# Optimization experiments

Measured on AMD Instinct MI355X. Metric: run time of the kernel, lower is better.

Reference implementation:

```python
import jax, jax.numpy as jnp
import numpy as np

NUM_EXPERTS = 8
NUM_ROWS = 1024
HIDDEN = 2048
INTER = 1024
TOPK = 2


def setup_inputs() -> dict:
    key = jax.random.key(0)
    kx, kr, k1, k2, k3 = jax.random.split(key, 5)
    x = jax.random.normal(kx, (NUM_ROWS, HIDDEN), dtype=jnp.float32)
    router_probs = jax.random.normal(kr, (NUM_ROWS, NUM_EXPERTS), dtype=jnp.float32)
    fc1 = jax.random.uniform(k1, (NUM_EXPERTS, HIDDEN, INTER), minval=-0.1, maxval=0.1, dtype=jnp.float32)
    fc2 = jax.random.uniform(k2, (NUM_EXPERTS, INTER, HIDDEN), minval=-0.1, maxval=0.1, dtype=jnp.float32)
    fc3 = jax.random.uniform(k3, (NUM_EXPERTS, HIDDEN, INTER), minval=-0.1, maxval=0.1, dtype=jnp.float32)
    return {"x": x, "router_probs": router_probs, "fc1": fc1, "fc2": fc2, "fc3": fc3}


def reference(x, router_probs, fc1, fc2, fc3):
    # Router: softmax over experts, top-k, renormalize
    router_softmax = jax.nn.softmax(router_probs.astype(jnp.float32), axis=1).astype(router_probs.dtype)
    topk_probs, topk_indices = jax.lax.top_k(router_softmax, TOPK)  # [N,K]
    topk_probs = topk_probs / jnp.sum(topk_probs, axis=1, keepdims=True)

    # Per-token combine weight for each expert: w[n,e] = sum_k prob[n,k]*[idx[n,k]==e]
    one_hot = jax.nn.one_hot(topk_indices, NUM_EXPERTS, dtype=x.dtype)  # [N,K,E]
    combine = jnp.einsum("nk,nke->ne", topk_probs, one_hot)  # [N,E]

    # Dense grouped GEMMs over all experts (reference form of dispatch/combine)
    h1 = jnp.einsum("nh,ehi->eni", x, fc1)  # [E,N,I]
    h3 = jnp.einsum("nh,ehi->eni", x, fc3)  # [E,N,I]
    act = jax.nn.silu(h1) * h3  # swiglu
    h2 = jnp.einsum("eni,eih->enh", act, fc2)  # [E,N,H]
    out = jnp.einsum("ne,enh->nh", combine, h2)  # [N,H]
    return out
```

## Files before the change

### kernel.cpp

```cpp
#include <hip/hip_runtime.h>

#define NEXP 8
#define NTOK 1024
#define HID 2048
#define ITR 1024

typedef __attribute__((ext_vector_type(8))) short short8;
typedef __attribute__((ext_vector_type(4))) float f32x4;

__device__ __forceinline__ unsigned short f2bf(float f) {
  unsigned u = __float_as_uint(f);
  u += 0x7fffu + ((u >> 16) & 1u);
  return (unsigned short)(u >> 16);
}

__device__ __forceinline__ void gl_lds16(const void* g, void* l) {
  __builtin_amdgcn_global_load_lds(
      (const __attribute__((address_space(1))) unsigned int*)g,
      (__attribute__((address_space(3))) unsigned int*)l, 16, 0, 0);
}

__global__ __launch_bounds__(256) void k_setup(const float* __restrict__ x,
                                               unsigned int* __restrict__ xb,
                                               float* __restrict__ out) {
  int i = blockIdx.x * 256 + threadIdx.x;
  f32x4 z = {0.f, 0.f, 0.f, 0.f};
  *(f32x4*)(out + (size_t)i * 4) = z;
  f32x4 v = *(const f32x4*)(x + (size_t)i * 4);
  xb[(size_t)i * 2] = (unsigned)f2bf(v[0]) | ((unsigned)f2bf(v[1]) << 16);
  xb[(size_t)i * 2 + 1] = (unsigned)f2bf(v[2]) | ((unsigned)f2bf(v[3]) << 16);
}

__global__ __launch_bounds__(1024) void k_router(const float* __restrict__ rp,
                                                 int* __restrict__ counts,
                                                 int* __restrict__ base,
                                                 int* __restrict__ toklist,
                                                 float* __restrict__ wlist) {
  __shared__ int c[NEXP];
  __shared__ int sb[NEXP];
  int n = threadIdx.x;
  if (n < NEXP) c[n] = 0;
  __syncthreads();
  float r[NEXP];
#pragma unroll
  for (int e = 0; e < NEXP; ++e) r[e] = rp[n * NEXP + e];
  int i1 = 0;
  float m1 = r[0];
#pragma unroll
  for (int e = 1; e < NEXP; ++e)
    if (r[e] > m1) { m1 = r[e]; i1 = e; }
  int i2 = -1;
  float m2 = -3.4e38f;
#pragma unroll
  for (int e = 0; e < NEXP; ++e)
    if (e != i1 && r[e] > m2) { m2 = r[e]; i2 = e; }
  float p1 = 1.f / (1.f + __expf(m2 - m1));
  float p2 = 1.f - p1;
  int s1 = atomicAdd(&c[i1], 1);
  int s2 = atomicAdd(&c[i2], 1);
  __syncthreads();
  if (n == 0) {
    int a = 0;
#pragma unroll
    for (int e = 0; e < NEXP; ++e) { sb[e] = a; a += c[e]; }
  }
  __syncthreads();
  int q1 = sb[i1] + s1;
  toklist[q1] = n; wlist[q1] = p1;
  int q2 = sb[i2] + s2;
  toklist[q2] = n; wlist[q2] = p2;
  if (n < NEXP) { counts[n] = c[n]; base[n] = sb[n]; }
}

__global__ __launch_bounds__(256) void k_transcvt(const float* __restrict__ in,
                                                  unsigned short* __restrict__ out,
                                                  int R, int C) {
  const int e = blockIdx.z;
  const float* src = in + (size_t)e * R * C;
  unsigned short* dst = out + (size_t)e * R * C;
  const int r0 = blockIdx.x * 64, c0 = blockIdx.y * 64;
  __shared__ unsigned short t[64][66];
  const int tid = threadIdx.x;
  const int r = tid >> 2, q = tid & 3;
  const float* p = src + (size_t)(r0 + r) * C + c0 + q * 4;
#pragma unroll
  for (int i = 0; i < 4; ++i) {
    f32x4 v = *(const f32x4*)(p + i * 16);
#pragma unroll
    for (int j = 0; j < 4; ++j) t[r][i * 16 + q * 4 + j] = f2bf(v[j]);
  }
  __syncthreads();
  const int cc = tid >> 2, rq = (tid & 3) * 16;
  unsigned short tmp[16];
#pragma unroll
  for (int i = 0; i < 16; ++i) tmp[i] = t[rq + i][cc];
  unsigned short* qo = dst + (size_t)(c0 + cc) * R + r0 + rq;
  *(short8*)qo = *(const short8*)tmp;
  *(short8*)(qo + 8) = *(const short8*)(tmp + 8);
}

__global__ __launch_bounds__(512, 4) void k_gemm13(
    const unsigned short* __restrict__ w1t, const unsigned short* __restrict__ w3t,
    const unsigned short* __restrict__ xb, const int* __restrict__ counts,
    const int* __restrict__ base, const int* __restrict__ toklist,
    unsigned short* __restrict__ act) {
  const int bid = blockIdx.x;
  const int e = bid & 7;
  const int t2 = bid >> 3;
  const int ntile = t2 & 31;
  const int mtile = t2 >> 5;
  const int cnt = counts[e];
  const int mbase = mtile * 256;
  if (mbase >= cnt) return;
  const int n0 = ntile * 32;
  const int rbase = base[e];

  __shared__ __align__(16) unsigned short lds[2 * 20480];
  const int tid = threadIdx.x;
  const int lane = tid & 63, w = tid >> 6;

  const unsigned short* srcA[4];
  int dofA[4];
#pragma unroll
  for (int i = 0; i < 4; ++i) {
    int c = i * 512 + tid;
    int r = c >> 3, b = c & 7;
    int row = mbase + r;
    int tok = toklist[rbase + ((row < cnt) ? row : (cnt - 1))];
    srcA[i] = xb + (size_t)tok * HID + (b ^ (r & 7)) * 8;
    dofA[i] = (i * 512 + w * 64) * 8;
  }
  const int mat = tid >> 8;
  const int cw = tid & 255;
  const int rw = cw >> 3, bw = cw & 7;
  const unsigned short* srcW =
      (mat ? w3t : w1t) + ((size_t)e * ITR + n0 + rw) * HID + (bw ^ (rw & 7)) * 8;
  const int dofW = 16384 + mat * 2048 + (w & 3) * 512;

  int offA[2][2], offW[2][2];
#pragma unroll
  for (int i = 0; i < 2; ++i)
#pragma unroll
    for (int s = 0; s < 2; ++s) {
      int kb = s * 4 + (lane >> 4);
      int rowA = w * 32 + i * 16 + (lane & 15);
      offA[i][s] = rowA * 128 + ((kb ^ (rowA & 7)) << 4);
      int rowW = i * 16 + (lane & 15);
      offW[i][s] = 32768 + rowW * 128 + ((kb ^ (rowW & 7)) << 4);
    }

  f32x4 acc1[2][2], acc3[2][2];
#pragma unroll
  for (int mi = 0; mi < 2; ++mi)
#pragma unroll
    for (int ni = 0; ni < 2; ++ni) {
      acc1[mi][ni] = (f32x4){0.f, 0.f, 0.f, 0.f};
      acc3[mi][ni] = (f32x4){0.f, 0.f, 0.f, 0.f};
    }

#define STG13(buf, kt)                                      \
  {                                                         \
    int k0 = (kt) * 64;                                     \
    unsigned short* Lb = lds + (buf) * 20480;               \
    _Pragma("unroll") for (int i = 0; i < 4; ++i)           \
        gl_lds16(srcA[i] + k0, Lb + dofA[i]);               \
    gl_lds16(srcW + k0, Lb + dofW);                         \
  }

  STG13(0, 0);
  __syncthreads();
  int buf = 0;
  for (int kt = 0; kt < HID / 64; ++kt) {
    if (kt + 1 < HID / 64) STG13(buf ^ 1, kt + 1);
    const char* Lb = (const char*)(lds + buf * 20480);
#pragma unroll
    for (int s = 0; s < 2; ++s) {
      short8 af[2], w1f[2], w3f[2];
#pragma unroll
      for (int mi = 0; mi < 2; ++mi) af[mi] = *(const short8*)(Lb + offA[mi][s]);
#pragma unroll
      for (int ni = 0; ni < 2; ++ni) {
        w1f[ni] = *(const short8*)(Lb + offW[ni][s]);
        w3f[ni] = *(const short8*)(Lb + offW[ni][s] + 4096);
      }
#pragma unroll
      for (int ni = 0; ni < 2; ++ni)
#pragma unroll
        for (int mi = 0; mi < 2; ++mi) {
          acc1[mi][ni] = __builtin_amdgcn_mfma_f32_16x16x32_bf16(
              af[mi], w1f[ni], acc1[mi][ni], 0, 0, 0);
          acc3[mi][ni] = __builtin_amdgcn_mfma_f32_16x16x32_bf16(
              af[mi], w3f[ni], acc3[mi][ni], 0, 0, 0);
        }
    }
    __syncthreads();
    buf ^= 1;
  }

  unsigned short* lact = lds;
#pragma unroll
  for (int mi = 0; mi < 2; ++mi)
#pragma unroll
    for (int ni = 0; ni < 2; ++ni)
#pragma unroll
      for (int rr = 0; rr < 4; ++rr) {
        float h1 = acc1[mi][ni][rr], h3 = acc3[mi][ni][rr];
        float a = h1 * (1.f / (1.f + __expf(-h1))) * h3;
        int row = w * 32 + mi * 16 + (lane >> 4) * 4 + rr;
        int col = ni * 16 + (lane & 15);
        lact[row * 40 + col] = f2bf(a);
      }
  __syncthreads();
#pragma unroll
  for (int p = 0; p < 2; ++p) {
    int row = p * 128 + (tid >> 2);
    int q = (tid & 3) * 8;
    if (mbase + row < cnt)
      *(short8*)(act + (size_t)(rbase + mbase + row) * ITR + n0 + q) =
          *(const short8*)&lact[row * 40 + q];
  }
}

__global__ __launch_bounds__(512, 4) void k_gemm2(
    const unsigned short* __restrict__ w2t, const unsigned short* __restrict__ act,
    const int* __restrict__ counts, const int* __restrict__ base,
    const int* __restrict__ toklist, const float* __restrict__ wlist,
    float* __restrict__ out) {
  const int bid = blockIdx.x;
  const int e = bid & 7;
  const int t2 = bid >> 3;
  const int ntile = t2 & 63;
  const int mtile = t2 >> 6;
  const int cnt = counts[e];
  const int mbase = mtile * 256;
  if (mbase >= cnt) return;
  const int n0 = ntile * 32;
  const int rbase = base[e];

  __shared__ __align__(16) unsigned short lds[2 * 18432];
  const int tid = threadIdx.x;
  const int lane = tid & 63, w = tid >> 6;

  const unsigned short* srcA[4];
  int dofA[4];
#pragma unroll
  for (int i = 0; i < 4; ++i) {
    int c = i * 512 + tid;
    int r = c >> 3, b = c & 7;
    int arow = rbase + mbase + r;
    if (arow > 2047) arow = 2047;
    srcA[i] = act + (size_t)arow * ITR + (b ^ (r & 7)) * 8;
    dofA[i] = (i * 512 + w * 64) * 8;
  }
  const int cw = tid & 255;
  const int rw = cw >> 3, bw = cw & 7;
  const unsigned short* srcW =
      w2t + ((size_t)e * HID + n0 + rw) * ITR + (bw ^ (rw & 7)) * 8;
  const int dofW = 16384 + (w & 3) * 512;

  int offA[2][2], offW[2][2];
#pragma unroll
  for (int i = 0; i < 2; ++i)
#pragma unroll
    for (int s = 0; s < 2; ++s) {
      int kb = s * 4 + (lane >> 4);
      int rowA = w * 32 + i * 16 + (lane & 15);
      offA[i][s] = rowA * 128 + ((kb ^ (rowA & 7)) << 4);
      int rowW = i * 16 + (lane & 15);
      offW[i][s] = 32768 + rowW * 128 + ((kb ^ (rowW & 7)) << 4);
    }

  f32x4 acc[2][2];
#pragma unroll
  for (int mi = 0; mi < 2; ++mi)
#pragma unroll
    for (int ni = 0; ni < 2; ++ni) acc[mi][ni] = (f32x4){0.f, 0.f, 0.f, 0.f};

#define STG2(buf, kt)                                       \
  {                                                         \
    int k0 = (kt) * 64;                                     \
    unsigned short* Lb = lds + (buf) * 18432;               \
    _Pragma("unroll") for (int i = 0; i < 4; ++i)           \
        gl_lds16(srcA[i] + k0, Lb + dofA[i]);               \
    if (w < 4) gl_lds16(srcW + k0, Lb + dofW);              \
  }

  STG2(0, 0);
  __syncthreads();
  int buf = 0;
  for (int kt = 0; kt < ITR / 64; ++kt) {
    if (kt + 1 < ITR / 64) STG2(buf ^ 1, kt + 1);
    const char* Lb = (const char*)(lds + buf * 18432);
#pragma unroll
    for (int s = 0; s < 2; ++s) {
      short8 af[2], wf[2];
#pragma unroll
      for (int mi = 0; mi < 2; ++mi) af[mi] = *(const short8*)(Lb + offA[mi][s]);
#pragma unroll
      for (int ni = 0; ni < 2; ++ni) wf[ni] = *(const short8*)(Lb + offW[ni][s]);
#pragma unroll
      for (int ni = 0; ni < 2; ++ni)
#pragma unroll
        for (int mi = 0; mi < 2; ++mi)
          acc[mi][ni] = __builtin_amdgcn_mfma_f32_16x16x32_bf16(
              af[mi], wf[ni], acc[mi][ni], 0, 0, 0);
    }
    __syncthreads();
    buf ^= 1;
  }

#pragma unroll
  for (int mi = 0; mi < 2; ++mi)
#pragma unroll
    for (int rr = 0; rr < 4; ++rr) {
      int lr = w * 32 + mi * 16 + (lane >> 4) * 4 + rr;
      int grow = mbase + lr;
      if (grow < cnt) {
        float pv = wlist[rbase + grow];
        int tok = toklist[rbase + grow];
        float* orow = out + (size_t)tok * HID + n0 + (lane & 15);
#pragma unroll
        for (int ni = 0; ni < 2; ++ni)
          atomicAdd(orow + ni * 16, acc[mi][ni][rr] * pv);
      }
    }
}

extern "C" void kernel_launch(void* const* d_in, const int* in_sizes, int n_in,
                              void* d_out, int out_size, void* d_ws,
                              size_t ws_size, hipStream_t stream) {
  (void)in_sizes; (void)n_in; (void)out_size; (void)ws_size;
  const float* x = (const float*)d_in[0];
  const float* rp = (const float*)d_in[1];
  const float* fc1 = (const float*)d_in[2];
  const float* fc2 = (const float*)d_in[3];
  const float* fc3 = (const float*)d_in[4];
  float* out = (float*)d_out;
  char* ws = (char*)d_ws;

  int* counts = (int*)ws;
  int* base = (int*)(ws + 256);
  int* toklist = (int*)(ws + 4096);
  float* wlist = (float*)(ws + 12288);
  unsigned short* xb = (unsigned short*)(ws + 32768);
  unsigned short* act = (unsigned short*)(ws + 4227072);
  unsigned short* w3t = (unsigned short*)(ws + 8421376);
  unsigned short* w12t = (unsigned short*)(ws + 41975808);

  k_setup<<<2048, 256, 0, stream>>>(x, (unsigned int*)xb, out);
  k_router<<<1, 1024, 0, stream>>>(rp, counts, base, toklist, wlist);
  k_transcvt<<<dim3(HID / 64, ITR / 64, NEXP), 256, 0, stream>>>(fc1, w12t, HID, ITR);
  k_transcvt<<<dim3(HID / 64, ITR / 64, NEXP), 256, 0, stream>>>(fc3, w3t, HID, ITR);
  k_gemm13<<<1024, 512, 0, stream>>>(w12t, w3t, xb, counts, base, toklist, act);
  k_transcvt<<<dim3(ITR / 64, HID / 64, NEXP), 256, 0, stream>>>(fc2, w12t, ITR, HID);
  k_gemm2<<<2048, 512, 0, stream>>>(w12t, act, counts, base, toklist, wlist, out);
}
```

Before: 295.6 us.

## Fuse fp32 weight transpose-convert into grouped GEMM staging loops

Removes the three separate transpose-and-convert kernels for fc1, fc2 and fc3. The GEMM kernels now load fp32 weights straight from global memory into registers, convert them to bf16 and write them transposed into swizzled LDS, with register prefetch one tile ahead. This drops a full extra read and write pass over all the expert weights. In exchange, weight loads become narrow 4-8 byte per-thread reads instead of 16-byte async LDS loads, and each GEMM block that shares a weight tile redoes the conversion.

```diff
diff --git a/kernel.cpp b/kernel.cpp
--- a/kernel.cpp
+++ b/kernel.cpp
@@ -6,7 +6,10 @@
 #define ITR 1024
 
 typedef __attribute__((ext_vector_type(8))) short short8;
+typedef __attribute__((ext_vector_type(4))) short short4v;
 typedef __attribute__((ext_vector_type(4))) float f32x4;
+typedef __attribute__((ext_vector_type(2))) float f32x2;
+typedef __attribute__((ext_vector_type(2))) unsigned uint2v;
 
 __device__ __forceinline__ unsigned short f2bf(float f) {
   unsigned u = __float_as_uint(f);
@@ -72,35 +75,8 @@
   if (n < NEXP) { counts[n] = c[n]; base[n] = sb[n]; }
 }
 
-__global__ __launch_bounds__(256) void k_transcvt(const float* __restrict__ in,
-                                                  unsigned short* __restrict__ out,
-                                                  int R, int C) {
-  const int e = blockIdx.z;
-  const float* src = in + (size_t)e * R * C;
-  unsigned short* dst = out + (size_t)e * R * C;
-  const int r0 = blockIdx.x * 64, c0 = blockIdx.y * 64;
-  __shared__ unsigned short t[64][66];
-  const int tid = threadIdx.x;
-  const int r = tid >> 2, q = tid & 3;
-  const float* p = src + (size_t)(r0 + r) * C + c0 + q * 4;
-#pragma unroll
-  for (int i = 0; i < 4; ++i) {
-    f32x4 v = *(const f32x4*)(p + i * 16);
-#pragma unroll
-    for (int j = 0; j < 4; ++j) t[r][i * 16 + q * 4 + j] = f2bf(v[j]);
-  }
-  __syncthreads();
-  const int cc = tid >> 2, rq = (tid & 3) * 16;
-  unsigned short tmp[16];
-#pragma unroll
-  for (int i = 0; i < 16; ++i) tmp[i] = t[rq + i][cc];
-  unsigned short* qo = dst + (size_t)(c0 + cc) * R + r0 + rq;
-  *(short8*)qo = *(const short8*)tmp;
-  *(short8*)(qo + 8) = *(const short8*)(tmp + 8);
-}
-
 __global__ __launch_bounds__(512, 4) void k_gemm13(
-    const unsigned short* __restrict__ w1t, const unsigned short* __restrict__ w3t,
+    const float* __restrict__ fc1, const float* __restrict__ fc3,
     const unsigned short* __restrict__ xb, const int* __restrict__ counts,
     const int* __restrict__ base, const int* __restrict__ toklist,
     unsigned short* __restrict__ act) {
@@ -112,7 +88,7 @@
   const int cnt = counts[e];
   const int mbase = mtile * 256;
   if (mbase >= cnt) return;
-  const int n0 = ntile * 32;
+  const int n0t = ntile * 32;
   const int rbase = base[e];
 
   __shared__ __align__(16) unsigned short lds[2 * 20480];
@@ -123,30 +99,44 @@
   int dofA[4];
 #pragma unroll
   for (int i = 0; i < 4; ++i) {
-    int c = i * 512 + tid;
-    int r = c >> 3, b = c & 7;
+    int cc = i * 512 + tid;
+    int r = cc >> 3, b = cc & 7;
     int row = mbase + r;
     int tok = toklist[rbase + ((row < cnt) ? row : (cnt - 1))];
     srcA[i] = xb + (size_t)tok * HID + (b ^ (r & 7)) * 8;
     dofA[i] = (i * 512 + w * 64) * 8;
   }
+
   const int mat = tid >> 8;
-  const int cw = tid & 255;
-  const int rw = cw >> 3, bw = cw & 7;
-  const unsigned short* srcW =
-      (mat ? w3t : w1t) + ((size_t)e * ITR + n0 + rw) * HID + (bw ^ (rw & 7)) * 8;
-  const int dofW = 16384 + mat * 2048 + (w & 3) * 512;
-
-  int offA[2][2], offW[2][2];
-#pragma unroll
-  for (int i = 0; i < 2; ++i)
+  const int c8 = tid & 255;
+  const int kq = c8 >> 4;
+  const int n0 = (c8 & 15) * 2;
+  const float* wsrc = (mat ? fc3 : fc1) + (size_t)e * HID * ITR +
+                      (size_t)(kq * 4) * ITR + n0t + n0;
+  int wrb[2];
+#pragma unroll
+  for (int t = 0; t < 2; ++t) {
+    int nn = n0 + t;
+    wrb[t] = 32768 + mat * 4096 + nn * 128 + ((kq ^ (nn & 15)) << 3);
+  }
+
+  int offA[2][2], woff[2][2][2];
+#pragma unroll
+  for (int mi = 0; mi < 2; ++mi)
 #pragma unroll
     for (int s = 0; s < 2; ++s) {
       int kb = s * 4 + (lane >> 4);
-      int rowA = w * 32 + i * 16 + (lane & 15);
-      offA[i][s] = rowA * 128 + ((kb ^ (rowA & 7)) << 4);
-      int rowW = i * 16 + (lane & 15);
-      offW[i][s] = 32768 + rowW * 128 + ((kb ^ (rowW & 7)) << 4);
+      int rowA = w * 32 + mi * 16 + (lane & 15);
+      offA[mi][s] = rowA * 128 + ((kb ^ (rowA & 7)) << 4);
+    }
+#pragma unroll
+  for (int ni = 0; ni < 2; ++ni)
+#pragma unroll
+    for (int s = 0; s < 2; ++s) {
+      int n = ni * 16 + (lane & 15);
+      int kb0 = s * 8 + (lane >> 4) * 2;
+      woff[ni][s][0] = n * 128 + ((kb0 ^ (n & 15)) << 3);
+      woff[ni][s][1] = n * 128 + (((kb0 + 1) ^ (n & 15)) << 3);
     }
 
   f32x4 acc1[2][2], acc3[2][2];
@@ -158,43 +148,76 @@
       acc3[mi][ni] = (f32x4){0.f, 0.f, 0.f, 0.f};
     }
 
-#define STG13(buf, kt)                                      \
-  {                                                         \
-    int k0 = (kt) * 64;                                     \
-    unsigned short* Lb = lds + (buf) * 20480;               \
-    _Pragma("unroll") for (int i = 0; i < 4; ++i)           \
-        gl_lds16(srcA[i] + k0, Lb + dofA[i]);               \
-    gl_lds16(srcW + k0, Lb + dofW);                         \
-  }
-
-  STG13(0, 0);
-  __syncthreads();
-  int buf = 0;
-  for (int kt = 0; kt < HID / 64; ++kt) {
-    if (kt + 1 < HID / 64) STG13(buf ^ 1, kt + 1);
-    const char* Lb = (const char*)(lds + buf * 20480);
-#pragma unroll
-    for (int s = 0; s < 2; ++s) {
-      short8 af[2], w1f[2], w3f[2];
-#pragma unroll
-      for (int mi = 0; mi < 2; ++mi) af[mi] = *(const short8*)(Lb + offA[mi][s]);
-#pragma unroll
-      for (int ni = 0; ni < 2; ++ni) {
-        w1f[ni] = *(const short8*)(Lb + offW[ni][s]);
-        w3f[ni] = *(const short8*)(Lb + offW[ni][s] + 4096);
-      }
-#pragma unroll
-      for (int ni = 0; ni < 2; ++ni)
-#pragma unroll
-        for (int mi = 0; mi < 2; ++mi) {
-          acc1[mi][ni] = __builtin_amdgcn_mfma_f32_16x16x32_bf16(
-              af[mi], w1f[ni], acc1[mi][ni], 0, 0, 0);
-          acc3[mi][ni] = __builtin_amdgcn_mfma_f32_16x16x32_bf16(
-              af[mi], w3f[ni], acc3[mi][ni], 0, 0, 0);
-        }
-    }
+  float wvA[8], wvB[8];
+
+#define STGA13(bb, kt)                                    \
+  {                                                       \
+    int k0 = (kt) * 64;                                   \
+    unsigned short* Lb = lds + (bb) * 20480;              \
+    _Pragma("unroll") for (int i = 0; i < 4; ++i)         \
+        gl_lds16(srcA[i] + k0, Lb + dofA[i]);             \
+  }
+#define LOADW13(wv, kt)                                   \
+  {                                                       \
+    const float* g = wsrc + (size_t)(kt) * 64 * ITR;      \
+    _Pragma("unroll") for (int j = 0; j < 4; ++j) {       \
+      f32x2 vv = *(const f32x2*)(g + (size_t)j * ITR);    \
+      wv[2 * j] = vv[0];                                  \
+      wv[2 * j + 1] = vv[1];                              \
+    }                                                     \
+  }
+#define CVTW13(wv, bb)                                                        \
+  {                                                                           \
+    _Pragma("unroll") for (int t = 0; t < 2; ++t) {                           \
+      unsigned lo = (unsigned)f2bf(wv[t]) | ((unsigned)f2bf(wv[2 + t]) << 16);\
+      unsigned hi =                                                           \
+          (unsigned)f2bf(wv[4 + t]) | ((unsigned)f2bf(wv[6 + t]) << 16);      \
+      uint2v v = {lo, hi};                                                    \
+      *(uint2v*)((char*)lds + (bb) * 40960 + wrb[t]) = v;                     \
+    }                                                                         \
+  }
+#define COMPUTE13(bb)                                                         \
+  {                                                                           \
+    const char* Lb = (const char*)lds + (bb) * 40960;                         \
+    _Pragma("unroll") for (int s = 0; s < 2; ++s) {                           \
+      short8 af[2];                                                           \
+      _Pragma("unroll") for (int mi = 0; mi < 2; ++mi)                        \
+          af[mi] = *(const short8*)(Lb + offA[mi][s]);                        \
+      _Pragma("unroll") for (int ni = 0; ni < 2; ++ni) {                      \
+        short4v l1 = *(const short4v*)(Lb + 32768 + woff[ni][s][0]);          \
+        short4v h1 = *(const short4v*)(Lb + 32768 + woff[ni][s][1]);          \
+        short4v l3 = *(const short4v*)(Lb + 36864 + woff[ni][s][0]);          \
+        short4v h3 = *(const short4v*)(Lb + 36864 + woff[ni][s][1]);          \
+        short8 w1f = __builtin_shufflevector(l1, h1, 0, 1, 2, 3, 4, 5, 6, 7); \
+        short8 w3f = __builtin_shufflevector(l3, h3, 0, 1, 2, 3, 4, 5, 6, 7); \
+        _Pragma("unroll") for (int mi = 0; mi < 2; ++mi) {                    \
+          acc1[mi][ni] = __builtin_amdgcn_mfma_f32_16x16x32_bf16(             \
+              af[mi], w1f, acc1[mi][ni], 0, 0, 0);                            \
+          acc3[mi][ni] = __builtin_amdgcn_mfma_f32_16x16x32_bf16(             \
+              af[mi], w3f, acc3[mi][ni], 0, 0, 0);                            \
+        }                                                                     \
+      }                                                                       \
+    }                                                                         \
+  }
+
+  LOADW13(wvA, 0);
+  STGA13(0, 0);
+  CVTW13(wvA, 0);
+  LOADW13(wvB, 1);
+  __syncthreads();
+  for (int kt = 0; kt < 32; kt += 2) {
+    STGA13(1, kt + 1);
+    CVTW13(wvB, 1);
+    if (kt + 2 < 32) LOADW13(wvA, kt + 2);
+    COMPUTE13(0);
     __syncthreads();
-    buf ^= 1;
+    if (kt + 2 < 32) {
+      STGA13(0, kt + 2);
+      CVTW13(wvA, 0);
+    }
+    if (kt + 3 < 32) LOADW13(wvB, kt + 3);
+    COMPUTE13(1);
+    __syncthreads();
   }
 
   unsigned short* lact = lds;
@@ -216,13 +239,13 @@
     int row = p * 128 + (tid >> 2);
     int q = (tid & 3) * 8;
     if (mbase + row < cnt)
-      *(short8*)(act + (size_t)(rbase + mbase + row) * ITR + n0 + q) =
+      *(short8*)(act + (size_t)(rbase + mbase + row) * ITR + n0t + q) =
           *(const short8*)&lact[row * 40 + q];
   }
 }
 
 __global__ __launch_bounds__(512, 4) void k_gemm2(
-    const unsigned short* __restrict__ w2t, const unsigned short* __restrict__ act,
+    const float* __restrict__ fc2, const unsigned short* __restrict__ act,
     const int* __restrict__ counts, const int* __restrict__ base,
     const int* __restrict__ toklist, const float* __restrict__ wlist,
     float* __restrict__ out) {
@@ -234,7 +257,7 @@
   const int cnt = counts[e];
   const int mbase = mtile * 256;
   if (mbase >= cnt) return;
-  const int n0 = ntile * 32;
+  const int n0t = ntile * 32;
   const int rbase = base[e];
 
   __shared__ __align__(16) unsigned short lds[2 * 18432];
@@ -245,29 +268,37 @@
   int dofA[4];
 #pragma unroll
   for (int i = 0; i < 4; ++i) {
-    int c = i * 512 + tid;
-    int r = c >> 3, b = c & 7;
+    int cc = i * 512 + tid;
+    int r = cc >> 3, b = cc & 7;
     int arow = rbase + mbase + r;
     if (arow > 2047) arow = 2047;
     srcA[i] = act + (size_t)arow * ITR + (b ^ (r & 7)) * 8;
     dofA[i] = (i * 512 + w * 64) * 8;
   }
-  const int cw = tid & 255;
-  const int rw = cw >> 3, bw = cw & 7;
-  const unsigned short* srcW =
-      w2t + ((size_t)e * HID + n0 + rw) * ITR + (bw ^ (rw & 7)) * 8;
-  const int dofW = 16384 + (w & 3) * 512;
-
-  int offA[2][2], offW[2][2];
-#pragma unroll
-  for (int i = 0; i < 2; ++i)
+
+  const int kq = tid >> 5;
+  const int n0 = tid & 31;
+  const float* wsrc =
+      fc2 + (size_t)e * ITR * HID + (size_t)(kq * 4) * HID + n0t + n0;
+  const int wrb = 32768 + n0 * 128 + ((kq ^ (n0 & 15)) << 3);
+
+  int offA[2][2], woff[2][2][2];
+#pragma unroll
+  for (int mi = 0; mi < 2; ++mi)
 #pragma unroll
     for (int s = 0; s < 2; ++s) {
       int kb = s * 4 + (lane >> 4);
-      int rowA = w * 32 + i * 16 + (lane & 15);
-      offA[i][s] = rowA * 128 + ((kb ^ (rowA & 7)) << 4);
-      int rowW = i * 16 + (lane & 15);
-      offW[i][s] = 32768 + rowW * 128 + ((kb ^ (rowW & 7)) << 4);
+      int rowA = w * 32 + mi * 16 + (lane & 15);
+      offA[mi][s] = rowA * 128 + ((kb ^ (rowA & 7)) << 4);
+    }
+#pragma unroll
+  for (int ni = 0; ni < 2; ++ni)
+#pragma unroll
+    for (int s = 0; s < 2; ++s) {
+      int n = ni * 16 + (lane & 15);
+      int kb0 = s * 8 + (lane >> 4) * 2;
+      woff[ni][s][0] = n * 128 + ((kb0 ^ (n & 15)) << 3);
+      woff[ni][s][1] = n * 128 + (((kb0 + 1) ^ (n & 15)) << 3);
     }
 
   f32x4 acc[2][2];
@@ -276,37 +307,64 @@
 #pragma unroll
     for (int ni = 0; ni < 2; ++ni) acc[mi][ni] = (f32x4){0.f, 0.f, 0.f, 0.f};
 
-#define STG2(buf, kt)                                       \
-  {                                                         \
-    int k0 = (kt) * 64;                                     \
-    unsigned short* Lb = lds + (buf) * 18432;               \
-    _Pragma("unroll") for (int i = 0; i < 4; ++i)           \
-        gl_lds16(srcA[i] + k0, Lb + dofA[i]);               \
-    if (w < 4) gl_lds16(srcW + k0, Lb + dofW);              \
-  }
-
-  STG2(0, 0);
-  __syncthreads();
-  int buf = 0;
-  for (int kt = 0; kt < ITR / 64; ++kt) {
-    if (kt + 1 < ITR / 64) STG2(buf ^ 1, kt + 1);
-    const char* Lb = (const char*)(lds + buf * 18432);
-#pragma unroll
-    for (int s = 0; s < 2; ++s) {
-      short8 af[2], wf[2];
-#pragma unroll
-      for (int mi = 0; mi < 2; ++mi) af[mi] = *(const short8*)(Lb + offA[mi][s]);
-#pragma unroll
-      for (int ni = 0; ni < 2; ++ni) wf[ni] = *(const short8*)(Lb + offW[ni][s]);
-#pragma unroll
-      for (int ni = 0; ni < 2; ++ni)
-#pragma unroll
-        for (int mi = 0; mi < 2; ++mi)
-          acc[mi][ni] = __builtin_amdgcn_mfma_f32_16x16x32_bf16(
-              af[mi], wf[ni], acc[mi][ni], 0, 0, 0);
-    }
+  float wvA[4], wvB[4];
+
+#define STGA2(bb, kt)                                     \
+  {                                                       \
+    int k0 = (kt) * 64;                                   \
+    unsigned short* Lb = lds + (bb) * 18432;              \
+    _Pragma("unroll") for (int i = 0; i < 4; ++i)         \
+        gl_lds16(srcA[i] + k0, Lb + dofA[i]);             \
+  }
+#define LOADW2(wv, kt)                                    \
+  {                                                       \
+    const float* g = wsrc + (size_t)(kt) * 64 * HID;      \
+    _Pragma("unroll") for (int j = 0; j < 4; ++j)         \
+        wv[j] = g[(size_t)j * HID];                       \
+  }
+#define CVTW2(wv, bb)                                                       \
+  {                                                                         \
+    unsigned lo = (unsigned)f2bf(wv[0]) | ((unsigned)f2bf(wv[1]) << 16);    \
+    unsigned hi = (unsigned)f2bf(wv[2]) | ((unsigned)f2bf(wv[3]) << 16);    \
+    uint2v v = {lo, hi};                                                    \
+    *(uint2v*)((char*)lds + (bb) * 36864 + wrb) = v;                        \
+  }
+#define COMPUTE2(bb)                                                          \
+  {                                                                           \
+    const char* Lb = (const char*)lds + (bb) * 36864;                         \
+    _Pragma("unroll") for (int s = 0; s < 2; ++s) {                           \
+      short8 af[2];                                                           \
+      _Pragma("unroll") for (int mi = 0; mi < 2; ++mi)                        \
+          af[mi] = *(const short8*)(Lb + offA[mi][s]);                        \
+      _Pragma("unroll") for (int ni = 0; ni < 2; ++ni) {                      \
+        short4v lw = *(const short4v*)(Lb + 32768 + woff[ni][s][0]);          \
+        short4v hw = *(const short4v*)(Lb + 32768 + woff[ni][s][1]);          \
+        short8 wf = __builtin_shufflevector(lw, hw, 0, 1, 2, 3, 4, 5, 6, 7);  \
+        _Pragma("unroll") for (int mi = 0; mi < 2; ++mi)                      \
+            acc[mi][ni] = __builtin_amdgcn_mfma_f32_16x16x32_bf16(            \
+                af[mi], wf, acc[mi][ni], 0, 0, 0);                            \
+      }                                                                       \
+    }                                                                         \
+  }
+
+  LOADW2(wvA, 0);
+  STGA2(0, 0);
+  CVTW2(wvA, 0);
+  LOADW2(wvB, 1);
+  __syncthreads();
+  for (int kt = 0; kt < 16; kt += 2) {
+    STGA2(1, kt + 1);
+    CVTW2(wvB, 1);
+    if (kt + 2 < 16) LOADW2(wvA, kt + 2);
+    COMPUTE2(0);
     __syncthreads();
-    buf ^= 1;
+    if (kt + 2 < 16) {
+      STGA2(0, kt + 2);
+      CVTW2(wvA, 0);
+    }
+    if (kt + 3 < 16) LOADW2(wvB, kt + 3);
+    COMPUTE2(1);
+    __syncthreads();
   }
 
 #pragma unroll
@@ -318,7 +376,7 @@
       if (grow < cnt) {
         float pv = wlist[rbase + grow];
         int tok = toklist[rbase + grow];
-        float* orow = out + (size_t)tok * HID + n0 + (lane & 15);
+        float* orow = out + (size_t)tok * HID + n0t + (lane & 15);
 #pragma unroll
         for (int ni = 0; ni < 2; ++ni)
           atomicAdd(orow + ni * 16, acc[mi][ni][rr] * pv);
@@ -344,14 +402,9 @@
   float* wlist = (float*)(ws + 12288);
   unsigned short* xb = (unsigned short*)(ws + 32768);
   unsigned short* act = (unsigned short*)(ws + 4227072);
-  unsigned short* w3t = (unsigned short*)(ws + 8421376);
-  unsigned short* w12t = (unsigned short*)(ws + 41975808);
 
   k_setup<<<2048, 256, 0, stream>>>(x, (unsigned int*)xb, out);
   k_router<<<1, 1024, 0, stream>>>(rp, counts, base, toklist, wlist);
-  k_transcvt<<<dim3(HID / 64, ITR / 64, NEXP), 256, 0, stream>>>(fc1, w12t, HID, ITR);
-  k_transcvt<<<dim3(HID / 64, ITR / 64, NEXP), 256, 0, stream>>>(fc3, w3t, HID, ITR);
-  k_gemm13<<<1024, 512, 0, stream>>>(w12t, w3t, xb, counts, base, toklist, act);
-  k_transcvt<<<dim3(ITR / 64, HID / 64, NEXP), 256, 0, stream>>>(fc2, w12t, ITR, HID);
-  k_gemm2<<<2048, 512, 0, stream>>>(w12t, act, counts, base, toklist, wlist, out);
-}
+  k_gemm13<<<1024, 512, 0, stream>>>(fc1, fc3, xb, counts, base, toklist, act);
+  k_gemm2<<<2048, 512, 0, stream>>>(fc2, act, counts, base, toklist, wlist, out);
+}
```

Result: faster. 282.6 us (-4.4%).
